# Kernel tuning notes

Measured on AMD Instinct MI355X. Metric: run time of the kernel, lower is better.

Reference implementation:

```python
import jax, jax.numpy as jnp
import numpy as np

EPS = 1e-6
K = 3
R_MIN, R_MAX = 0.5, 2.0


def setup_inputs() -> dict:
    key = jax.random.key(0)
    k0, k1, k2, k3 = jax.random.split(key, 4)
    N, C, D, H, W = 2, 32, 48, 48, 48
    T = 1 + K + 3 + 1  # num_tokens = 6
    x = jax.random.normal(k0, (N, C, D, H, W), jnp.float32)
    w_field = jax.random.normal(k1, (4 * K, C), jnp.float32) * 0.05
    b_field = jnp.zeros((4 * K,), jnp.float32)
    gates = jax.random.normal(k2, (T,), jnp.float32)
    w_mix = jax.random.normal(k3, (C, T * C), jnp.float32) * 0.02
    b_mix = jnp.zeros((C,), jnp.float32)
    return {"x": x, "w_field": w_field, "b_field": b_field, "gates": gates, "w_mix": w_mix, "b_mix": b_mix}


def _reflect(coord, size):
    # torch 'reflection' padding, align_corners=False: reflect over [-0.5, size-0.5]
    c = jnp.abs(coord + 0.5)
    m = jnp.mod(c, 2.0 * size)
    return jnp.minimum(m, 2.0 * size - m) - 0.5


def _trilinear_sample(vol, gx, gy, gz):
    # vol: (N, D, H, W, C) channels-last; gx/gy/gz: (N, K, D, H, W) normalized coords in [-1, 1]
    N, D, H, W, C = vol.shape

    def unnorm(g, size):
        return _reflect(((g + 1.0) * size - 1.0) * 0.5, float(size))

    ix, iy, iz = unnorm(gx, W), unnorm(gy, H), unnorm(gz, D)
    x0 = jnp.floor(ix); y0 = jnp.floor(iy); z0 = jnp.floor(iz)
    fx = (ix - x0)[..., None]; fy = (iy - y0)[..., None]; fz = (iz - z0)[..., None]
    x0i = jnp.clip(x0.astype(jnp.int32), 0, W - 1); x1i = jnp.clip(x0i + 1, 0, W - 1)
    y0i = jnp.clip(y0.astype(jnp.int32), 0, H - 1); y1i = jnp.clip(y0i + 1, 0, H - 1)
    z0i = jnp.clip(z0.astype(jnp.int32), 0, D - 1); z1i = jnp.clip(z0i + 1, 0, D - 1)
    n = jnp.arange(N).reshape(N, 1, 1, 1, 1)

    def g(zi, yi, xi):
        return vol[n, zi, yi, xi]  # (N, K, D, H, W, C)

    c00 = g(z0i, y0i, x0i) * (1.0 - fx) + g(z0i, y0i, x1i) * fx
    c01 = g(z0i, y1i, x0i) * (1.0 - fx) + g(z0i, y1i, x1i) * fx
    c10 = g(z1i, y0i, x0i) * (1.0 - fx) + g(z1i, y0i, x1i) * fx
    c11 = g(z1i, y1i, x0i) * (1.0 - fx) + g(z1i, y1i, x1i) * fx
    c0 = c00 * (1.0 - fy) + c01 * fy
    c1 = c10 * (1.0 - fy) + c11 * fy
    return c0 * (1.0 - fz) + c1 * fz


def reference(x, w_field, b_field, gates, w_mix, b_mix):
    N, C, D, H, W = x.shape
    # field head: 1x1x1 conv C -> 4K, split into K unit directions U and radii r
    f = jnp.einsum('ncdhw,oc->nodhw', x, w_field) + b_field[None, :, None, None, None]
    f = f.reshape(N, K, 4, D, H, W)
    v = f[:, :, :3]
    U = v / jnp.sqrt(jnp.sum(v * v, axis=2, keepdims=True) + EPS)  # (N,K,3,D,H,W)
    r_s = R_MIN + (R_MAX - R_MIN) * jax.nn.sigmoid(f[:, :, 3])     # (N,K,D,H,W)
    # base grid, align_corners=False normalized coordinates
    gz0 = ((jnp.arange(D, dtype=x.dtype) + 0.5) * 2.0 / D - 1.0)[:, None, None]
    gy0 = ((jnp.arange(H, dtype=x.dtype) + 0.5) * 2.0 / H - 1.0)[None, :, None]
    gx0 = ((jnp.arange(W, dtype=x.dtype) + 0.5) * 2.0 / W - 1.0)[None, None, :]
    ux, uy, uz = U[:, :, 0], U[:, :, 1], U[:, :, 2]
    dx = 2.0 * r_s * ux / (W + EPS)
    dy = 2.0 * r_s * uy / (H + EPS)
    dz = 2.0 * r_s * uz / (D + EPS)
    vol = jnp.transpose(x, (0, 2, 3, 4, 1))  # (N,D,H,W,C)
    xp = _trilinear_sample(vol, gx0 + dx, gy0 + dy, gz0 + dz)  # (N,K,D,H,W,C)
    xm = _trilinear_sample(vol, gx0 - dx, gy0 - dy, gz0 - dz)
    xp = jnp.transpose(xp, (0, 1, 5, 2, 3, 4))  # (N,K,C,D,H,W)
    xm = jnp.transpose(xm, (0, 1, 5, 2, 3, 4))
    a = 0.5 * (xp + xm)
    o = 0.5 * (xp - xm)
    inv_r = 1.0 / (jax.lax.stop_gradient(r_s) + EPS)  # r detached in original
    d1 = o * inv_r[:, :, None]                        # (N,K,C,D,H,W)
    G = jnp.einsum('nkadhw,nkcdhw->nacdhw', U, d1)     # (N,3,C,D,H,W)
    d2 = (xp + xm - 2.0 * x[:, None]) * (inv_r * inv_r)[:, :, None]
    L = d2.mean(axis=1)                                # (N,C,D,H,W)
    tokens = jnp.concatenate([x[:, None], a, G, L[:, None]], axis=1)  # (N,T,C,D,H,W)
    T = tokens.shape[1]
    gated = tokens * jax.nn.sigmoid(gates)[None, :, None, None, None, None]
    delta = jnp.einsum('nmdhw,om->nodhw', gated.reshape(N, T * C, D, H, W), w_mix)
    delta = delta + b_mix[None, :, None, None, None]
    return x + delta
```

## Files before the change

### kernel.cpp

```cpp
#include <hip/hip_runtime.h>
#include <math.h>

#define NB   2
#define CH   32
#define DHW  (48*48*48)
#define TT   8
#define EPSF 1e-6f

#define TILE_N   1521
#define TILE_WSTR 1522
#define GROUPS   8

#define TOK_OFF  0
#define TOK_STR  64
#define TILE_OFF 16384
#define SMEM_SZ  40736

#define WS_BT_F 0
#define WS_WF   4096
#define WS_BF   4480
#define WS_BM   4492

typedef __attribute__((ext_vector_type(8))) short short8;
typedef __attribute__((ext_vector_type(8))) _Float16 half8;
typedef __attribute__((ext_vector_type(4))) float floatx4;
typedef __attribute__((ext_vector_type(2))) _Float16 h2;

struct __align__(8) q4 { h2 lo, hi; };

__device__ __forceinline__ h2 pkrtz(float a, float b) {
    return __builtin_bit_cast(h2, __builtin_amdgcn_cvt_pkrtz(a, b));
}
__device__ __forceinline__ unsigned pkrtz_u(float a, float b) {
    return __builtin_bit_cast(unsigned, __builtin_amdgcn_cvt_pkrtz(a, b));
}

__global__ __launch_bounds__(256) void prep_kernel(
        const float* __restrict__ w_field,
        const float* __restrict__ b_field,
        const float* __restrict__ gates,
        const float* __restrict__ w_mix,
        const float* __restrict__ b_mix,
        float* __restrict__ ws) {
    int i = blockIdx.x * 256 + threadIdx.x;
    {
        int o = i >> 8, k = i & 255, c = k >> 3, t = k & 7;
        float sg = 1.0f / (1.0f + expf(-gates[t]));
        _Float16 hv = (_Float16)(sg * w_mix[o * 256 + t * 32 + c]);
        ((unsigned short*)(ws + WS_BT_F))[o * 256 + k] = __builtin_bit_cast(unsigned short, hv);
    }
    if (i < 384) { int c = i / 12, o = i - c * 12; ws[WS_WF + i] = w_field[o * 32 + c]; }
    if (i < 12)  ws[WS_BF + i] = b_field[i];
    if (i < 32)  ws[WS_BM + i] = b_mix[i];
}

__global__ __launch_bounds__(256) void geo_main(
        const float* __restrict__ x,
        const float* __restrict__ ws,
        float* __restrict__ out) {
    __shared__ __align__(16) char smem[SMEM_SZ];
    char* tokb  = smem + TOK_OFF;
    q4*   tileq = (q4*)(smem + TILE_OFF);
    float* cbuf = (float*)smem;

    const int tid = threadIdx.x;
    const int lin = (blockIdx.x & 7) * 108 + (blockIdx.x >> 3);
    const int bx = lin % 6, by = (lin / 6) % 6, bz = (lin / 36) % 12, n = lin / 432;
    const int lx = tid & 7, ly = (tid >> 3) & 7, lz = tid >> 6;
    const int w = bx * 8 + lx, h = by * 8 + ly, d = bz * 4 + lz;
    const int xlo = bx * 8 - 2, ylo = by * 8 - 2, zlo = bz * 4 - 2;
    const int lane = tid & 63, w64 = tid & 192;

    const float* xn = x + (size_t)n * CH * DHW;

    int goff[6];
#pragma unroll
    for (int i = 0; i < 6; ++i) {
        int e  = tid + i * 256;
        int ee = (e < TILE_N) ? e : 0;
        int tz = ee / 169; int r0 = ee - tz * 169;
        int ty = r0 / 13;  int tx = r0 - ty * 13;
        int zg = min(max(zlo + tz, 0), 47);
        int yg = min(max(ylo + ty, 0), 47);
        int xg = min(max(xlo + tx, 0), 47);
        goff[i] = (zg * 48 + yg) * 48 + xg;
    }

    const int pos = (d * 48 + h) * 48 + w;
    float f[12];
#pragma unroll
    for (int o = 0; o < 12; ++o) f[o] = ws[WS_BF + o];
    for (int c = 0; c < CH; ++c) {
        float xv = xn[c * DHW + pos];
        const float* wf = ws + WS_WF + c * 12;
#pragma unroll
        for (int o = 0; o < 12; ++o) f[o] = fmaf(wf[o], xv, f[o]);
    }

    h2 fx2[6], fy2[6], fz2[6];
    int a00[6], a01[6], a10[6], a11[6];
    float uxk[3], uyk[3], uzk[3], irk[3], ir2k[3];
    const float cscale = 48.0f / (48.0f + EPSF);
#pragma unroll
    for (int k = 0; k < 3; ++k) {
        float vx = f[4*k], vy = f[4*k+1], vz = f[4*k+2], s = f[4*k+3];
        float inv = 1.0f / sqrtf(vx*vx + vy*vy + vz*vz + EPSF);
        float ux = vx * inv, uy = vy * inv, uz = vz * inv;
        float r  = 0.5f + 1.5f / (1.0f + expf(-s));
        uxk[k] = ux; uyk[k] = uy; uzk[k] = uz;
        float ir = 1.0f / (r + EPSF); irk[k] = ir; ir2k[k] = ir * ir;
#pragma unroll
        for (int sgn = 0; sgn < 2; ++sgn) {
            int   si = 2 * k + sgn;
            float sf = sgn ? -1.0f : 1.0f;
            float txr = (float)w + sf * r * ux * cscale;
            float tyr = (float)h + sf * r * uy * cscale;
            float tzr = (float)d + sf * r * uz * cscale;
            float cx = fabsf(txr + 0.5f); float ix = fminf(cx, 96.0f - cx) - 0.5f;
            float cy = fabsf(tyr + 0.5f); float iy = fminf(cy, 96.0f - cy) - 0.5f;
            float cz = fabsf(tzr + 0.5f); float iz = fminf(cz, 96.0f - cz) - 0.5f;
            float x0f = floorf(ix), y0f = floorf(iy), z0f = floorf(iz);
            float fx = ix - x0f, fy = iy - y0f, fz = iz - z0f;
            int x0 = min(max((int)x0f, 0), 47); int x1 = min(x0 + 1, 47);
            int y0 = min(max((int)y0f, 0), 47); int y1 = min(y0 + 1, 47);
            int z0 = min(max((int)z0f, 0), 47); int z1 = min(z0 + 1, 47);
            float fxe = (x1 == x0) ? 0.0f : fx;
            _Float16 hx = (_Float16)fxe, hy = (_Float16)fy, hz = (_Float16)fz;
            fx2[si] = (h2){hx, hx}; fy2[si] = (h2){hy, hy}; fz2[si] = (h2){hz, hz};
            int lz0 = z0 - zlo, lz1 = z1 - zlo;
            int ly0 = y0 - ylo, ly1 = y1 - ylo;
            int lx0 = x0 - xlo;
            a00[si] = (lz0 * 13 + ly0) * 13 + lx0;
            a01[si] = (lz0 * 13 + ly1) * 13 + lx0;
            a10[si] = (lz1 * 13 + ly0) * 13 + lx0;
            a11[si] = (lz1 * 13 + ly1) * 13 + lx0;
        }
    }

    if (tid == 0) {
        q4 z; z.lo = (h2){0, 0}; z.hi = (h2){0, 0};
        tileq[TILE_N] = z; tileq[TILE_WSTR + TILE_N] = z;
    }
    {
        float ld[24];
#pragma unroll
        for (int cg = 0; cg < 4; ++cg) {
            const float* xc = xn + cg * DHW;
#pragma unroll
            for (int i = 0; i < 6; ++i) ld[cg * 6 + i] = xc[goff[i]];
        }
#pragma unroll
        for (int i = 0; i < 6; ++i) {
            int e = tid + i * 256;
            if (e < TILE_N) {
                q4 vq; vq.lo = pkrtz(ld[i], ld[6 + i]); vq.hi = pkrtz(ld[12 + i], ld[18 + i]);
                tileq[e] = vq;
            }
        }
    }

    q4 pqv[6];
    {
        float l2[24];
#pragma unroll
        for (int cg = 0; cg < 4; ++cg) {
            const float* xc = xn + (4 + cg) * DHW;
#pragma unroll
            for (int i = 0; i < 6; ++i) l2[cg * 6 + i] = xc[goff[i]];
        }
#pragma unroll
        for (int i = 0; i < 6; ++i) {
            pqv[i].lo = pkrtz(l2[i], l2[6 + i]);
            pqv[i].hi = pkrtz(l2[12 + i], l2[18 + i]);
        }
    }
    __syncthreads();

    floatx4 acc[4][2];
#pragma unroll
    for (int mt = 0; mt < 4; ++mt)
#pragma unroll
        for (int nt = 0; nt < 2; ++nt) acc[mt][nt] = (floatx4){0.f, 0.f, 0.f, 0.f};

    const int self = ((lz + 2) * 13 + (ly + 2)) * 13 + (lx + 2);
    const unsigned short* bt = (const unsigned short*)(ws + WS_BT_F);
    const int tokq = (tid >> 3) & 3;
    const int qm = lane >> 4, nlo = lane & 15;

    short8 bc0 = *(const short8*)(bt + (nlo * 256 + qm * 8));
    short8 bc1 = *(const short8*)(bt + ((nlo + 16) * 256 + qm * 8));

    for (int g = 0; g < GROUPS; ++g) {
        const int rb = (g & 1);
        const int wb = rb ^ 1;
        if (g < GROUPS - 1) {
#pragma unroll
            for (int i = 0; i < 6; ++i) {
                int e = tid + i * 256;
                if (e < TILE_N) tileq[wb * TILE_WSTR + e] = pqv[i];
            }
        }
        float nld[24];
        if (g < GROUPS - 2) {
            const float* xg = xn + (g + 2) * 4 * DHW;
#pragma unroll
            for (int cg = 0; cg < 4; ++cg) {
                const float* xc = xg + cg * DHW;
#pragma unroll
                for (int i = 0; i < 6; ++i) nld[cg * 6 + i] = xc[goff[i]];
            }
        }
        short8 bn0 = bc0, bn1 = bc1;
        if (g < GROUPS - 1) {
            bn0 = *(const short8*)(bt + (nlo * 256 + (g + 1) * 32 + qm * 8));
            bn1 = *(const short8*)(bt + ((nlo + 16) * 256 + (g + 1) * 32 + qm * 8));
        }
        const q4* tb = tileq + rb * TILE_WSTR;
        q4 s2 = tb[self];
        q4 vv[6];
#pragma unroll
        for (int si = 0; si < 6; ++si) {
            int b00 = a00[si], b01 = a01[si], b10 = a10[si], b11 = a11[si];
            q4 v000 = tb[b00], v001 = tb[b00 + 1];
            q4 v010 = tb[b01], v011 = tb[b01 + 1];
            q4 v100 = tb[b10], v101 = tb[b10 + 1];
            q4 v110 = tb[b11], v111 = tb[b11 + 1];
            h2 fx = fx2[si], fy = fy2[si], fz = fz2[si];
            h2 c00l = v000.lo + fx * (v001.lo - v000.lo);
            h2 c00h = v000.hi + fx * (v001.hi - v000.hi);
            h2 c01l = v010.lo + fx * (v011.lo - v010.lo);
            h2 c01h = v010.hi + fx * (v011.hi - v010.hi);
            h2 c10l = v100.lo + fx * (v101.lo - v100.lo);
            h2 c10h = v100.hi + fx * (v101.hi - v100.hi);
            h2 c11l = v110.lo + fx * (v111.lo - v110.lo);
            h2 c11h = v110.hi + fx * (v111.hi - v110.hi);
            h2 c0l = c00l + fy * (c01l - c00l);
            h2 c0h = c00h + fy * (c01h - c00h);
            h2 c1l = c10l + fy * (c11l - c10l);
            h2 c1h = c10h + fy * (c11h - c10h);
            vv[si].lo = c0l + fz * (c1l - c0l);
            vv[si].hi = c0h + fz * (c1h - c0h);
        }
#pragma unroll
        for (int sub = 0; sub < 4; ++sub) {
            float xv = (sub == 0) ? (float)s2.lo.x : (sub == 1) ? (float)s2.lo.y
                     : (sub == 2) ? (float)s2.hi.x : (float)s2.hi.y;
            float val[6];
#pragma unroll
            for (int si = 0; si < 6; ++si)
                val[si] = (sub == 0) ? (float)vv[si].lo.x : (sub == 1) ? (float)vv[si].lo.y
                        : (sub == 2) ? (float)vv[si].hi.x : (float)vv[si].hi.y;
            float t1, t2, t3, gx, gy, gz, l;
            {
                float sp, sm, d1;
                sp = val[0]; sm = val[1]; t1 = 0.5f * (sp + sm);
                d1 = 0.5f * (sp - sm) * irk[0];
                gx = uxk[0] * d1; gy = uyk[0] * d1; gz = uzk[0] * d1;
                l  = (sp + sm - 2.0f * xv) * ir2k[0];
                sp = val[2]; sm = val[3]; t2 = 0.5f * (sp + sm);
                d1 = 0.5f * (sp - sm) * irk[1];
                gx = fmaf(uxk[1], d1, gx); gy = fmaf(uyk[1], d1, gy); gz = fmaf(uzk[1], d1, gz);
                l  = fmaf(sp + sm - 2.0f * xv, ir2k[1], l);
                sp = val[4]; sm = val[5]; t3 = 0.5f * (sp + sm);
                d1 = 0.5f * (sp - sm) * irk[2];
                gx = fmaf(uxk[2], d1, gx); gy = fmaf(uyk[2], d1, gy); gz = fmaf(uzk[2], d1, gz);
                l  = fmaf(sp + sm - 2.0f * xv, ir2k[2], l);
            }
            uint4 tw;
            tw.x = pkrtz_u(xv, t1);
            tw.y = pkrtz_u(t2, t3);
            tw.z = pkrtz_u(gx, gy);
            tw.w = pkrtz_u(gz, l * (1.0f / 3.0f));
            int qe = sub ^ tokq;
            *(uint4*)(tokb + tid * TOK_STR + qe * 16) = tw;
        }
        {
            half8 hb0 = __builtin_bit_cast(half8, bc0);
            half8 hb1 = __builtin_bit_cast(half8, bc1);
#pragma unroll
            for (int mt = 0; mt < 4; ++mt) {
                int row = w64 + mt * 16 + nlo;
                int qe  = qm ^ ((row >> 3) & 3);
                half8 a = __builtin_bit_cast(half8,
                          *(const short8*)(tokb + row * TOK_STR + qe * 16));
                acc[mt][0] = __builtin_amdgcn_mfma_f32_16x16x32_f16(a, hb0, acc[mt][0], 0, 0, 0);
                acc[mt][1] = __builtin_amdgcn_mfma_f32_16x16x32_f16(a, hb1, acc[mt][1], 0, 0, 0);
            }
        }
        bc0 = bn0; bc1 = bn1;

        if (g < GROUPS - 2) {
#pragma unroll
            for (int i = 0; i < 6; ++i) {
                pqv[i].lo = pkrtz(nld[i], nld[6 + i]);
                pqv[i].hi = pkrtz(nld[12 + i], nld[18 + i]);
            }
        }
        __syncthreads();
    }

    {
#pragma unroll
        for (int mt = 0; mt < 4; ++mt)
#pragma unroll
            for (int nt = 0; nt < 2; ++nt)
#pragma unroll
                for (int r = 0; r < 4; ++r) {
                    int vr = w64 + mt * 16 + qm * 4 + r;
                    int col = nt * 16 + nlo;
                    cbuf[vr * 36 + (col ^ (vr & 31))] = acc[mt][nt][r];
                }
    }
    __syncthreads();

    const float* dr = cbuf + tid * 36;
    float* on = out + (size_t)n * CH * DHW;
#pragma unroll
    for (int o = 0; o < 32; ++o)
        __builtin_nontemporal_store(
            xn[o * DHW + pos] + dr[o ^ (tid & 31)] + ws[WS_BM + o],
            on + o * DHW + pos);
}

extern "C" void kernel_launch(void* const* d_in, const int* in_sizes, int n_in,
                              void* d_out, int out_size, void* d_ws, size_t ws_size,
                              hipStream_t stream) {
    const float *x = (const float*)d_in[0], *w_field = (const float*)d_in[1],
                *b_field = (const float*)d_in[2], *gates = (const float*)d_in[3],
                *w_mix = (const float*)d_in[4], *b_mix = (const float*)d_in[5];
    for (int i = 0; i < n_in; ++i) {
        switch (in_sizes[i]) {
            case NB * CH * DHW: x       = (const float*)d_in[i]; break;
            case 12 * CH:       w_field = (const float*)d_in[i]; break;
            case 12:            b_field = (const float*)d_in[i]; break;
            case TT:            gates   = (const float*)d_in[i]; break;
            case CH * TT * CH:  w_mix   = (const float*)d_in[i]; break;
            case CH:            b_mix   = (const float*)d_in[i]; break;
            default: break;
        }
    }
    float* ws = (float*)d_ws;
    prep_kernel<<<32, 256, 0, stream>>>(w_field, b_field, gates, w_mix, b_mix, ws);
    geo_main<<<864, 256, 0, stream>>>(x, ws, (float*)d_out);
}
```

Measured before the change: 154.6 us.

## Process eight channels per pipeline stage with 16-byte LDS gathers

Widens each halo tile entry from 4 to 8 fp16 channels, so the channel loop runs 4 groups instead of 8 with half as many barriers. Each trilinear gather now fetches 16 bytes per corner, amortizing LDS address math and instruction issue over twice the channels. Each group also issues two MFMA batches. The cost is double the LDS tile footprint (about 65KB total, which may reduce blocks per CU) and double the registers for the prefetch buffers (48 floats plus 6 q8v), raising the risk of lower occupancy or register spills.

```diff
diff --git a/kernel.cpp b/kernel.cpp
--- a/kernel.cpp
+++ b/kernel.cpp
@@ -9,12 +9,13 @@
 
 #define TILE_N   1521
 #define TILE_WSTR 1522
-#define GROUPS   8
+#define TILE_BYTES (TILE_WSTR*16)
+#define GROUPS   4
 
 #define TOK_OFF  0
 #define TOK_STR  64
 #define TILE_OFF 16384
-#define SMEM_SZ  40736
+#define SMEM_SZ  (16384 + 2*TILE_BYTES)
 
 #define WS_BT_F 0
 #define WS_WF   4096
@@ -26,13 +27,19 @@
 typedef __attribute__((ext_vector_type(4))) float floatx4;
 typedef __attribute__((ext_vector_type(2))) _Float16 h2;
 
-struct __align__(8) q4 { h2 lo, hi; };
+struct __align__(16) q8v { h2 q[4]; };
 
 __device__ __forceinline__ h2 pkrtz(float a, float b) {
     return __builtin_bit_cast(h2, __builtin_amdgcn_cvt_pkrtz(a, b));
 }
 __device__ __forceinline__ unsigned pkrtz_u(float a, float b) {
     return __builtin_bit_cast(unsigned, __builtin_amdgcn_cvt_pkrtz(a, b));
+}
+__device__ __forceinline__ q8v ldq8(const char* p) {
+    return __builtin_bit_cast(q8v, *(const half8*)p);
+}
+__device__ __forceinline__ void stq8(char* p, q8v v) {
+    *(half8*)p = __builtin_bit_cast(half8, v);
 }
 
 __global__ __launch_bounds__(256) void prep_kernel(
@@ -60,7 +67,7 @@
         float* __restrict__ out) {
     __shared__ __align__(16) char smem[SMEM_SZ];
     char* tokb  = smem + TOK_OFF;
-    q4*   tileq = (q4*)(smem + TILE_OFF);
+    char* tileb = smem + TILE_OFF;
     float* cbuf = (float*)smem;
 
     const int tid = threadIdx.x;
@@ -138,13 +145,14 @@
     }
 
     if (tid == 0) {
-        q4 z; z.lo = (h2){0, 0}; z.hi = (h2){0, 0};
-        tileq[TILE_N] = z; tileq[TILE_WSTR + TILE_N] = z;
+        q8v z; z.q[0] = (h2){0,0}; z.q[1] = (h2){0,0}; z.q[2] = (h2){0,0}; z.q[3] = (h2){0,0};
+        stq8(tileb + TILE_N * 16, z);
+        stq8(tileb + TILE_BYTES + TILE_N * 16, z);
     }
     {
-        float ld[24];
-#pragma unroll
-        for (int cg = 0; cg < 4; ++cg) {
+        float ld[48];
+#pragma unroll
+        for (int cg = 0; cg < 8; ++cg) {
             const float* xc = xn + cg * DHW;
 #pragma unroll
             for (int i = 0; i < 6; ++i) ld[cg * 6 + i] = xc[goff[i]];
@@ -153,25 +161,31 @@
         for (int i = 0; i < 6; ++i) {
             int e = tid + i * 256;
             if (e < TILE_N) {
-                q4 vq; vq.lo = pkrtz(ld[i], ld[6 + i]); vq.hi = pkrtz(ld[12 + i], ld[18 + i]);
-                tileq[e] = vq;
-            }
-        }
-    }
-
-    q4 pqv[6];
+                q8v vq;
+                vq.q[0] = pkrtz(ld[i],      ld[6  + i]);
+                vq.q[1] = pkrtz(ld[12 + i], ld[18 + i]);
+                vq.q[2] = pkrtz(ld[24 + i], ld[30 + i]);
+                vq.q[3] = pkrtz(ld[36 + i], ld[42 + i]);
+                stq8(tileb + e * 16, vq);
+            }
+        }
+    }
+
+    q8v pqv[6];
     {
-        float l2[24];
-#pragma unroll
-        for (int cg = 0; cg < 4; ++cg) {
-            const float* xc = xn + (4 + cg) * DHW;
+        float l2[48];
+#pragma unroll
+        for (int cg = 0; cg < 8; ++cg) {
+            const float* xc = xn + (8 + cg) * DHW;
 #pragma unroll
             for (int i = 0; i < 6; ++i) l2[cg * 6 + i] = xc[goff[i]];
         }
 #pragma unroll
         for (int i = 0; i < 6; ++i) {
-            pqv[i].lo = pkrtz(l2[i], l2[6 + i]);
-            pqv[i].hi = pkrtz(l2[12 + i], l2[18 + i]);
+            pqv[i].q[0] = pkrtz(l2[i],      l2[6  + i]);
+            pqv[i].q[1] = pkrtz(l2[12 + i], l2[18 + i]);
+            pqv[i].q[2] = pkrtz(l2[24 + i], l2[30 + i]);
+            pqv[i].q[3] = pkrtz(l2[36 + i], l2[42 + i]);
         }
     }
     __syncthreads();
@@ -187,8 +201,10 @@
     const int tokq = (tid >> 3) & 3;
     const int qm = lane >> 4, nlo = lane & 15;
 
-    short8 bc0 = *(const short8*)(bt + (nlo * 256 + qm * 8));
-    short8 bc1 = *(const short8*)(bt + ((nlo + 16) * 256 + qm * 8));
+    short8 bcA0 = *(const short8*)(bt + (nlo * 256 + 0 * 32 + qm * 8));
+    short8 bcA1 = *(const short8*)(bt + ((nlo + 16) * 256 + 0 * 32 + qm * 8));
+    short8 bcB0 = *(const short8*)(bt + (nlo * 256 + 1 * 32 + qm * 8));
+    short8 bcB1 = *(const short8*)(bt + ((nlo + 16) * 256 + 1 * 32 + qm * 8));
 
     for (int g = 0; g < GROUPS; ++g) {
         const int rb = (g & 1);
@@ -197,103 +213,108 @@
 #pragma unroll
             for (int i = 0; i < 6; ++i) {
                 int e = tid + i * 256;
-                if (e < TILE_N) tileq[wb * TILE_WSTR + e] = pqv[i];
-            }
-        }
-        float nld[24];
+                if (e < TILE_N) stq8(tileb + wb * TILE_BYTES + e * 16, pqv[i]);
+            }
+        }
+        float nld[48];
         if (g < GROUPS - 2) {
-            const float* xg = xn + (g + 2) * 4 * DHW;
-#pragma unroll
-            for (int cg = 0; cg < 4; ++cg) {
+            const float* xg = xn + (g + 2) * 8 * DHW;
+#pragma unroll
+            for (int cg = 0; cg < 8; ++cg) {
                 const float* xc = xg + cg * DHW;
 #pragma unroll
                 for (int i = 0; i < 6; ++i) nld[cg * 6 + i] = xc[goff[i]];
             }
         }
-        short8 bn0 = bc0, bn1 = bc1;
+        short8 bnA0 = bcA0, bnA1 = bcA1, bnB0 = bcB0, bnB1 = bcB1;
         if (g < GROUPS - 1) {
-            bn0 = *(const short8*)(bt + (nlo * 256 + (g + 1) * 32 + qm * 8));
-            bn1 = *(const short8*)(bt + ((nlo + 16) * 256 + (g + 1) * 32 + qm * 8));
-        }
-        const q4* tb = tileq + rb * TILE_WSTR;
-        q4 s2 = tb[self];
-        q4 vv[6];
+            int cc = 2 * (g + 1);
+            bnA0 = *(const short8*)(bt + (nlo * 256 + cc * 32 + qm * 8));
+            bnA1 = *(const short8*)(bt + ((nlo + 16) * 256 + cc * 32 + qm * 8));
+            bnB0 = *(const short8*)(bt + (nlo * 256 + (cc + 1) * 32 + qm * 8));
+            bnB1 = *(const short8*)(bt + ((nlo + 16) * 256 + (cc + 1) * 32 + qm * 8));
+        }
+        const char* tb = tileb + rb * TILE_BYTES;
+        q8v s2 = ldq8(tb + self * 16);
+        q8v vv[6];
 #pragma unroll
         for (int si = 0; si < 6; ++si) {
             int b00 = a00[si], b01 = a01[si], b10 = a10[si], b11 = a11[si];
-            q4 v000 = tb[b00], v001 = tb[b00 + 1];
-            q4 v010 = tb[b01], v011 = tb[b01 + 1];
-            q4 v100 = tb[b10], v101 = tb[b10 + 1];
-            q4 v110 = tb[b11], v111 = tb[b11 + 1];
+            q8v v000 = ldq8(tb + b00 * 16), v001 = ldq8(tb + b00 * 16 + 16);
+            q8v v010 = ldq8(tb + b01 * 16), v011 = ldq8(tb + b01 * 16 + 16);
+            q8v v100 = ldq8(tb + b10 * 16), v101 = ldq8(tb + b10 * 16 + 16);
+            q8v v110 = ldq8(tb + b11 * 16), v111 = ldq8(tb + b11 * 16 + 16);
             h2 fx = fx2[si], fy = fy2[si], fz = fz2[si];
-            h2 c00l = v000.lo + fx * (v001.lo - v000.lo);
-            h2 c00h = v000.hi + fx * (v001.hi - v000.hi);
-            h2 c01l = v010.lo + fx * (v011.lo - v010.lo);
-            h2 c01h = v010.hi + fx * (v011.hi - v010.hi);
-            h2 c10l = v100.lo + fx * (v101.lo - v100.lo);
-            h2 c10h = v100.hi + fx * (v101.hi - v100.hi);
-            h2 c11l = v110.lo + fx * (v111.lo - v110.lo);
-            h2 c11h = v110.hi + fx * (v111.hi - v110.hi);
-            h2 c0l = c00l + fy * (c01l - c00l);
-            h2 c0h = c00h + fy * (c01h - c00h);
-            h2 c1l = c10l + fy * (c11l - c10l);
-            h2 c1h = c10h + fy * (c11h - c10h);
-            vv[si].lo = c0l + fz * (c1l - c0l);
-            vv[si].hi = c0h + fz * (c1h - c0h);
-        }
-#pragma unroll
-        for (int sub = 0; sub < 4; ++sub) {
-            float xv = (sub == 0) ? (float)s2.lo.x : (sub == 1) ? (float)s2.lo.y
-                     : (sub == 2) ? (float)s2.hi.x : (float)s2.hi.y;
-            float val[6];
-#pragma unroll
-            for (int si = 0; si < 6; ++si)
-                val[si] = (sub == 0) ? (float)vv[si].lo.x : (sub == 1) ? (float)vv[si].lo.y
-                        : (sub == 2) ? (float)vv[si].hi.x : (float)vv[si].hi.y;
-            float t1, t2, t3, gx, gy, gz, l;
+#pragma unroll
+            for (int qd = 0; qd < 4; ++qd) {
+                h2 c00 = v000.q[qd] + fx * (v001.q[qd] - v000.q[qd]);
+                h2 c01 = v010.q[qd] + fx * (v011.q[qd] - v010.q[qd]);
+                h2 c10 = v100.q[qd] + fx * (v101.q[qd] - v100.q[qd]);
+                h2 c11 = v110.q[qd] + fx * (v111.q[qd] - v110.q[qd]);
+                h2 c0  = c00 + fy * (c01 - c00);
+                h2 c1  = c10 + fy * (c11 - c10);
+                vv[si].q[qd] = c0 + fz * (c1 - c0);
+            }
+        }
+#pragma unroll
+        for (int p = 0; p < 2; ++p) {
+#pragma unroll
+            for (int j = 0; j < 4; ++j) {
+                const int ce = p * 4 + j;
+                float xv = (ce & 1) ? (float)s2.q[ce >> 1].y : (float)s2.q[ce >> 1].x;
+                float val[6];
+#pragma unroll
+                for (int si = 0; si < 6; ++si)
+                    val[si] = (ce & 1) ? (float)vv[si].q[ce >> 1].y : (float)vv[si].q[ce >> 1].x;
+                float t1, t2, t3, gx, gy, gz, l;
+                {
+                    float sp, sm, d1;
+                    sp = val[0]; sm = val[1]; t1 = 0.5f * (sp + sm);
+                    d1 = 0.5f * (sp - sm) * irk[0];
+                    gx = uxk[0] * d1; gy = uyk[0] * d1; gz = uzk[0] * d1;
+                    l  = (sp + sm - 2.0f * xv) * ir2k[0];
+                    sp = val[2]; sm = val[3]; t2 = 0.5f * (sp + sm);
+                    d1 = 0.5f * (sp - sm) * irk[1];
+                    gx = fmaf(uxk[1], d1, gx); gy = fmaf(uyk[1], d1, gy); gz = fmaf(uzk[1], d1, gz);
+                    l  = fmaf(sp + sm - 2.0f * xv, ir2k[1], l);
+                    sp = val[4]; sm = val[5]; t3 = 0.5f * (sp + sm);
+                    d1 = 0.5f * (sp - sm) * irk[2];
+                    gx = fmaf(uxk[2], d1, gx); gy = fmaf(uyk[2], d1, gy); gz = fmaf(uzk[2], d1, gz);
+                    l  = fmaf(sp + sm - 2.0f * xv, ir2k[2], l);
+                }
+                uint4 tw;
+                tw.x = pkrtz_u(xv, t1);
+                tw.y = pkrtz_u(t2, t3);
+                tw.z = pkrtz_u(gx, gy);
+                tw.w = pkrtz_u(gz, l * (1.0f / 3.0f));
+                int qe = j ^ tokq;
+                *(uint4*)(tokb + tid * TOK_STR + qe * 16) = tw;
+            }
             {
-                float sp, sm, d1;
-                sp = val[0]; sm = val[1]; t1 = 0.5f * (sp + sm);
-                d1 = 0.5f * (sp - sm) * irk[0];
-                gx = uxk[0] * d1; gy = uyk[0] * d1; gz = uzk[0] * d1;
-                l  = (sp + sm - 2.0f * xv) * ir2k[0];
-                sp = val[2]; sm = val[3]; t2 = 0.5f * (sp + sm);
-                d1 = 0.5f * (sp - sm) * irk[1];
-                gx = fmaf(uxk[1], d1, gx); gy = fmaf(uyk[1], d1, gy); gz = fmaf(uzk[1], d1, gz);
-                l  = fmaf(sp + sm - 2.0f * xv, ir2k[1], l);
-                sp = val[4]; sm = val[5]; t3 = 0.5f * (sp + sm);
-                d1 = 0.5f * (sp - sm) * irk[2];
-                gx = fmaf(uxk[2], d1, gx); gy = fmaf(uyk[2], d1, gy); gz = fmaf(uzk[2], d1, gz);
-                l  = fmaf(sp + sm - 2.0f * xv, ir2k[2], l);
-            }
-            uint4 tw;
-            tw.x = pkrtz_u(xv, t1);
-            tw.y = pkrtz_u(t2, t3);
-            tw.z = pkrtz_u(gx, gy);
-            tw.w = pkrtz_u(gz, l * (1.0f / 3.0f));
-            int qe = sub ^ tokq;
-            *(uint4*)(tokb + tid * TOK_STR + qe * 16) = tw;
-        }
-        {
-            half8 hb0 = __builtin_bit_cast(half8, bc0);
-            half8 hb1 = __builtin_bit_cast(half8, bc1);
-#pragma unroll
-            for (int mt = 0; mt < 4; ++mt) {
-                int row = w64 + mt * 16 + nlo;
-                int qe  = qm ^ ((row >> 3) & 3);
-                half8 a = __builtin_bit_cast(half8,
-                          *(const short8*)(tokb + row * TOK_STR + qe * 16));
-                acc[mt][0] = __builtin_amdgcn_mfma_f32_16x16x32_f16(a, hb0, acc[mt][0], 0, 0, 0);
-                acc[mt][1] = __builtin_amdgcn_mfma_f32_16x16x32_f16(a, hb1, acc[mt][1], 0, 0, 0);
-            }
-        }
-        bc0 = bn0; bc1 = bn1;
+                short8 b0 = p ? bcB0 : bcA0;
+                short8 b1 = p ? bcB1 : bcA1;
+                half8 hb0 = __builtin_bit_cast(half8, b0);
+                half8 hb1 = __builtin_bit_cast(half8, b1);
+#pragma unroll
+                for (int mt = 0; mt < 4; ++mt) {
+                    int row = w64 + mt * 16 + nlo;
+                    int qe  = qm ^ ((row >> 3) & 3);
+                    half8 a = __builtin_bit_cast(half8,
+                              *(const short8*)(tokb + row * TOK_STR + qe * 16));
+                    acc[mt][0] = __builtin_amdgcn_mfma_f32_16x16x32_f16(a, hb0, acc[mt][0], 0, 0, 0);
+                    acc[mt][1] = __builtin_amdgcn_mfma_f32_16x16x32_f16(a, hb1, acc[mt][1], 0, 0, 0);
+                }
+            }
+        }
+        bcA0 = bnA0; bcA1 = bnA1; bcB0 = bnB0; bcB1 = bnB1;
 
         if (g < GROUPS - 2) {
 #pragma unroll
             for (int i = 0; i < 6; ++i) {
-                pqv[i].lo = pkrtz(nld[i], nld[6 + i]);
-                pqv[i].hi = pkrtz(nld[12 + i], nld[18 + i]);
+                pqv[i].q[0] = pkrtz(nld[i],      nld[6  + i]);
+                pqv[i].q[1] = pkrtz(nld[12 + i], nld[18 + i]);
+                pqv[i].q[2] = pkrtz(nld[24 + i], nld[30 + i]);
+                pqv[i].q[3] = pkrtz(nld[36 + i], nld[42 + i]);
             }
         }
         __syncthreads();
```

New measurement: 179.2 us. +15.9%, slower.
